# Kernel optimization log

Measured on AMD Instinct MI355X. Metric: run time of the kernel, lower is better.

Reference implementation:

```python
import jax, jax.numpy as jnp
import numpy as np

B, T, D_IN, HID, D_OUT = 16, 4096, 256, 512, 256


def setup_inputs() -> dict:
    key = jax.random.key(0)
    k0, k1, k2, k3 = jax.random.split(key, 4)
    x = jax.random.normal(k0, (B, T, D_IN), dtype=jnp.float32)
    # nn.Linear default init ~ U(-1/sqrt(fan_in), 1/sqrt(fan_in)); approximate with scaled normal
    W_in = jax.random.normal(k1, (HID, D_IN), dtype=jnp.float32) / np.sqrt(D_IN)
    # hidden_ff.weight is explicitly set to diag(rand(hid_dim)) in the module
    W_h = jnp.diag(jax.random.uniform(k2, (HID,), dtype=jnp.float32))
    W_out = jax.random.normal(k3, (D_OUT, HID), dtype=jnp.float32) / np.sqrt(HID)
    return {"x": x, "W_in": W_in, "W_h": W_h, "W_out": W_out}


def reference(x, W_in, W_h, W_out):
    # x: [B, T, D_in]; W_in: [H, D_in]; W_h: [H, H]; W_out: [D_out, H]
    xp = jnp.einsum('btd,hd->bth', x, W_in)  # input projection, [B, T, H]

    def step(h, xt):
        # h_t = x_t + h_{t-1} @ W_h^T  (linear recurrence, h_0 = 0)
        h_next = xt + h @ W_h.T
        return h_next, h_next

    h0 = jnp.zeros((x.shape[0], W_h.shape[0]), dtype=x.dtype)
    _, hs = jax.lax.scan(step, h0, jnp.swapaxes(xp, 0, 1))  # hs: [T, B, H]
    hs = jnp.swapaxes(hs, 0, 1)  # [B, T, H]
    return jnp.einsum('bth,oh->bto', hs, W_out)  # [B, T, D_out]
```

## Files before the change

### kernel.cpp

```cpp
#include <hip/hip_runtime.h>
#include <hip/hip_bf16.h>
#include <stdint.h>

#define BATCH 16
#define SEQT  4096
#define DIN   256
#define HID   512
#define DOUT  256
#define M_TOT 65536
#define CLEN  128
#define NCHUNK 32

typedef short bf16x8 __attribute__((ext_vector_type(8)));
typedef float f32x4  __attribute__((ext_vector_type(4)));
typedef unsigned short u16;
typedef unsigned short u16x4 __attribute__((ext_vector_type(4)));
typedef unsigned int uint32;

__device__ __forceinline__ void ld_lds16(const void* g, void* l) {
    __builtin_amdgcn_global_load_lds(
        (const __attribute__((address_space(1))) void*)g,
        (__attribute__((address_space(3))) void*)l, 16, 0, 0);
}

__device__ __forceinline__ u16 f2bf_rne(float f) {
    uint32 v = __float_as_uint(f);
    v += 0x7FFFu + ((v >> 16) & 1u);
    return (u16)(v >> 16);
}

__device__ __forceinline__ float bf2f(u16 s) {
    return __uint_as_float((uint32)s << 16);
}

__device__ __forceinline__ void splitf(float f, u16& hi, u16& lo) {
    const uint32 u = __float_as_uint(f);
    hi = (u16)(u >> 16);
    lo = f2bf_rne(f - __uint_as_float(u & 0xFFFF0000u));
}

__global__ __launch_bounds__(256) void prep(
        const float* __restrict__ Wh, const float* __restrict__ Win,
        const float* __restrict__ Wout, float* __restrict__ wdiag,
        float* __restrict__ wpow, u16* __restrict__ Winhi,
        u16* __restrict__ Winlo, u16* __restrict__ Wouthi,
        u16* __restrict__ Woutlo) {
    const int bid = blockIdx.x, tid = threadIdx.x;
    if (bid == 0) {
        for (int h = tid; h < HID; h += 256) {
            const float wv = Wh[(size_t)h * HID + h];
            wdiag[h] = wv;
            float p = 1.f;
            for (int t = 0; t < CLEN; ++t) { p *= wv; wpow[t * HID + h] = p; }
        }
    } else if (bid <= 128) {
        const int f4 = (bid - 1) * 256 + tid;
        const f32x4 v = *(const f32x4*)(Win + (size_t)f4 * 4);
        u16x4 hv, lv;
#pragma unroll
        for (int k = 0; k < 4; ++k) { u16 a, b; splitf(v[k], a, b); hv[k] = a; lv[k] = b; }
        *(u16x4*)(Winhi + (size_t)f4 * 4) = hv;
        *(u16x4*)(Winlo + (size_t)f4 * 4) = lv;
    } else {
        const int f4 = (bid - 129) * 256 + tid;
        const f32x4 v = *(const f32x4*)(Wout + (size_t)f4 * 4);
        u16x4 hv, lv;
#pragma unroll
        for (int k = 0; k < 4; ++k) { u16 a, b; splitf(v[k], a, b); hv[k] = a; lv[k] = b; }
        *(u16x4*)(Wouthi + (size_t)f4 * 4) = hv;
        *(u16x4*)(Woutlo + (size_t)f4 * 4) = lv;
    }
}

__global__ __launch_bounds__(256, 2) void gemm1_scan(
        const float* __restrict__ X, const u16* __restrict__ Whi,
        const u16* __restrict__ Wlo, u16* __restrict__ localbf,
        float* __restrict__ L, const float* __restrict__ wdiag) {
    __shared__ __align__(16) char smem[66048];
    u16*   Ah  = (u16*)smem;
    u16*   Al  = (u16*)(smem + 16384);
    u16*   Bh  = (u16*)(smem + 32768);
    u16*   Bl  = (u16*)(smem + 49152);
    u16*   stb = (u16*)smem;
    float* xw  = (float*)(smem + 65536);

    const int tid  = threadIdx.x;
    const int w    = tid >> 6;
    const int lane = tid & 63;

    const int bid  = blockIdx.x;
    const int xcd  = bid & 7;
    const int slot = bid >> 3;
    const int mBase = (xcd * 64 + (slot >> 2)) * 128;
    const int nBase = (slot & 3) * 128;

    const int wr = w >> 1, wc = w & 1;
    const int fr = lane & 15;
    const int kg = lane >> 4;

    const int bRow = lane >> 3;
    const int bCol = ((lane & 7) ^ bRow) * 8;

    f32x4 acc[4][4];
#pragma unroll
    for (int i = 0; i < 4; ++i)
#pragma unroll
        for (int j = 0; j < 4; ++j) acc[i][j] = (f32x4){0.f, 0.f, 0.f, 0.f};

    for (int k0 = 0; k0 < DIN; k0 += 64) {
#pragma unroll
        for (int i = 0; i < 4; ++i) {
            const int c = w * 4 + i;
            const int r = c * 8 + bRow;
            ld_lds16(Whi + (size_t)(nBase + r) * DIN + k0 + bCol, Bh + c * 512);
            ld_lds16(Wlo + (size_t)(nBase + r) * DIN + k0 + bCol, Bl + c * 512);
        }
#pragma unroll
        for (int it = 0; it < 4; ++it) {
            const int idx = it * 256 + tid;
            const int r  = idx >> 3;
            const int gl = idx & 7;
            const float* src = X + (size_t)(mBase + r) * DIN + k0 + gl * 8;
            const f32x4 v0 = *(const f32x4*)(src);
            const f32x4 v1 = *(const f32x4*)(src + 4);
            bf16x8 h8, l8;
#pragma unroll
            for (int e = 0; e < 4; ++e) {
                u16 a, b;
                splitf(v0[e], a, b); h8[e] = (short)a; l8[e] = (short)b;
                splitf(v1[e], a, b); h8[e + 4] = (short)a; l8[e + 4] = (short)b;
            }
            const int phys = r * 64 + ((gl ^ (r & 7)) * 8);
            *(bf16x8*)(Ah + phys) = h8;
            *(bf16x8*)(Al + phys) = l8;
        }
        __syncthreads();
#pragma unroll
        for (int ks = 0; ks < 2; ++ks) {
            const int colE = ks * 32 + kg * 8;
            bf16x8 ah[4], al[4], bh[4], bl[4];
#pragma unroll
            for (int f = 0; f < 4; ++f) {
                const int ra = wr * 64 + f * 16 + fr;
                const int pa = ra * 64 + (colE ^ ((fr & 7) << 3));
                ah[f] = *(const bf16x8*)(Ah + pa);
                al[f] = *(const bf16x8*)(Al + pa);
                const int rb = wc * 64 + f * 16 + fr;
                const int pb = rb * 64 + (colE ^ ((fr & 7) << 3));
                bh[f] = *(const bf16x8*)(Bh + pb);
                bl[f] = *(const bf16x8*)(Bl + pb);
            }
#pragma unroll
            for (int i = 0; i < 4; ++i)
#pragma unroll
                for (int j = 0; j < 4; ++j) {
                    acc[i][j] = __builtin_amdgcn_mfma_f32_16x16x32_bf16(ah[i], bh[j], acc[i][j], 0, 0, 0);
                    acc[i][j] = __builtin_amdgcn_mfma_f32_16x16x32_bf16(ah[i], bl[j], acc[i][j], 0, 0, 0);
                    acc[i][j] = __builtin_amdgcn_mfma_f32_16x16x32_bf16(al[i], bh[j], acc[i][j], 0, 0, 0);
                }
        }
        __syncthreads();
    }

    float w1[4], w2[4], w3[4], w4[4], w8[4], w16[4];
#pragma unroll
    for (int j = 0; j < 4; ++j) {
        const float wv = wdiag[nBase + wc * 64 + j * 16 + fr];
        w1[j] = wv; w2[j] = wv * wv; w3[j] = w2[j] * wv; w4[j] = w2[j] * w2[j];
        w8[j] = w4[j] * w4[j]; w16[j] = w8[j] * w8[j];
    }
    float Bst[4] = {0.f, 0.f, 0.f, 0.f};
#pragma unroll
    for (int i = 0; i < 4; ++i) {
#pragma unroll
        for (int j = 0; j < 4; ++j) {
            const float l0 = acc[i][j][0];
            const float l1 = fmaf(w1[j], l0, acc[i][j][1]);
            const float l2 = fmaf(w1[j], l1, acc[i][j][2]);
            const float l3 = fmaf(w1[j], l2, acc[i][j][3]);
            const float x0 = __shfl(l3, fr);
            const float x1 = __shfl(l3, fr + 16);
            const float x2 = __shfl(l3, fr + 32);
            const float x3 = __shfl(l3, fr + 48);
            float s = Bst[j];
            float S = s;
            s = fmaf(w4[j], s, x0); S = (kg == 1) ? s : S;
            s = fmaf(w4[j], s, x1); S = (kg == 2) ? s : S;
            s = fmaf(w4[j], s, x2); S = (kg == 3) ? s : S;
            s = fmaf(w4[j], s, x3);
            Bst[j] = s;
            acc[i][j][0] = fmaf(w1[j], S, l0);
            acc[i][j][1] = fmaf(w2[j], S, l1);
            acc[i][j][2] = fmaf(w3[j], S, l2);
            acc[i][j][3] = fmaf(w4[j], S, l3);
        }
    }
    if (wr == 0 && kg == 0) {
#pragma unroll
        for (int j = 0; j < 4; ++j) xw[wc * 64 + j * 16 + fr] = Bst[j];
    }
    __syncthreads();
    if (wr == 1) {
        const int cI = (mBase >> 7) & (NCHUNK - 1);
        const int bI = mBase >> 12;
#pragma unroll
        for (int j = 0; j < 4; ++j) {
            const float cin = xw[wc * 64 + j * 16 + fr];
            float wkg = 1.f;
            if (kg & 1) wkg *= w4[j];
            if (kg & 2) wkg *= w8[j];
            float f = wkg;
#pragma unroll
            for (int i = 0; i < 4; ++i) {
                const float g = f * cin;
                acc[i][j][0] = fmaf(w1[j], g, acc[i][j][0]);
                acc[i][j][1] = fmaf(w2[j], g, acc[i][j][1]);
                acc[i][j][2] = fmaf(w3[j], g, acc[i][j][2]);
                acc[i][j][3] = fmaf(w4[j], g, acc[i][j][3]);
                f *= w16[j];
            }
            if (kg == 0) {
                const float w32 = w16[j] * w16[j];
                const float w64 = w32 * w32;
                L[(cI * BATCH + bI) * HID + nBase + wc * 64 + j * 16 + fr]
                    = fmaf(w64, cin, Bst[j]);
            }
        }
    }
#pragma unroll
    for (int i = 0; i < 4; ++i)
#pragma unroll
        for (int j = 0; j < 4; ++j)
#pragma unroll
            for (int rg = 0; rg < 4; ++rg)
                stb[(wr * 64 + i * 16 + kg * 4 + rg) * 132
                    + wc * 64 + j * 16 + fr] = f2bf_rne(acc[i][j][rg]);
    __syncthreads();

    {
        const int rr2 = tid >> 4;
        const int cl  = (tid & 15) * 8;
#pragma unroll
        for (int p = 0; p < 8; ++p) {
            const int row = p * 16 + rr2;
            const bf16x8 v = *(const bf16x8*)(stb + row * 132 + cl);
            *(bf16x8*)(localbf + (size_t)(mBase + row) * HID + nBase + cl) = v;
        }
    }
}

__global__ __launch_bounds__(256) void scan_carry(
        const float* __restrict__ L, const float* __restrict__ wpow,
        float* __restrict__ carry) {
    const int idx = blockIdx.x * 256 + threadIdx.x;
    const int h = idx & (HID - 1);
    const int b = idx >> 9;
    const float wf = wpow[(CLEN - 1) * HID + h];
    float H = 0.f;
    for (int c = 0; c < NCHUNK; ++c) {
        const int o = (c * BATCH + b) * HID + h;
        carry[o] = H;
        H = fmaf(wf, H, L[o]);
    }
}

__global__ __launch_bounds__(256, 2) void gemm2_fix(
        const u16* __restrict__ localbf, const u16* __restrict__ Bhi_g,
        const u16* __restrict__ Blo_g, const float* __restrict__ wpow,
        const float* __restrict__ carry, float* __restrict__ C) {
    __shared__ __align__(16) char smem[65536];
    u16* Ah = (u16*)smem;
    u16* Al = (u16*)(smem + 16384);
    u16* Bh = (u16*)(smem + 32768);
    u16* Bl = (u16*)(smem + 49152);

    const int tid  = threadIdx.x;
    const int w    = tid >> 6;
    const int lane = tid & 63;

    const int bid  = blockIdx.x;
    const int xcd  = bid & 7;
    const int slot = bid >> 3;
    const int mBase = (xcd * 64 + (slot >> 1)) * 128;
    const int nBase = (slot & 1) * 128;

    const int wr = w >> 1, wc = w & 1;
    const int fr = lane & 15;
    const int kg = lane >> 4;

    const int bRow = lane >> 3;
    const int bCol = ((lane & 7) ^ bRow) * 8;

    const int cI = (mBase >> 7) & (NCHUNK - 1);
    const int bI = mBase >> 12;
    const float* crow = carry + (size_t)(cI * BATCH + bI) * HID;

    f32x4 acc[4][4];
#pragma unroll
    for (int i = 0; i < 4; ++i)
#pragma unroll
        for (int j = 0; j < 4; ++j) acc[i][j] = (f32x4){0.f, 0.f, 0.f, 0.f};

    for (int k0 = 0; k0 < HID; k0 += 64) {
#pragma unroll
        for (int i = 0; i < 4; ++i) {
            const int c = w * 4 + i;
            const int r2 = c * 8 + bRow;
            ld_lds16(Bhi_g + (size_t)(nBase + r2) * HID + k0 + bCol, Bh + c * 512);
            ld_lds16(Blo_g + (size_t)(nBase + r2) * HID + k0 + bCol, Bl + c * 512);
        }
#pragma unroll
        for (int it = 0; it < 4; ++it) {
            const int idx = it * 256 + tid;
            const int r  = idx >> 3;
            const int gl = idx & 7;
            const int gm = mBase + r;
            const size_t col = (size_t)(k0 + gl * 8);
            const bf16x8 lv = *(const bf16x8*)(localbf + (size_t)gm * HID + col);
            const f32x4 p0 = *(const f32x4*)(wpow + (size_t)r * HID + col);
            const f32x4 p1 = *(const f32x4*)(wpow + (size_t)r * HID + col + 4);
            const f32x4 c0 = *(const f32x4*)(crow + col);
            const f32x4 c1 = *(const f32x4*)(crow + col + 4);
            bf16x8 h8, l8;
#pragma unroll
            for (int e = 0; e < 4; ++e) {
                const float f0 = fmaf(p0[e], c0[e], bf2f((u16)lv[e]));
                const float f1 = fmaf(p1[e], c1[e], bf2f((u16)lv[e + 4]));
                u16 a, b;
                splitf(f0, a, b); h8[e] = (short)a; l8[e] = (short)b;
                splitf(f1, a, b); h8[e + 4] = (short)a; l8[e + 4] = (short)b;
            }
            const int phys = r * 64 + ((gl ^ (r & 7)) * 8);
            *(bf16x8*)(Ah + phys) = h8;
            *(bf16x8*)(Al + phys) = l8;
        }
        __syncthreads();
#pragma unroll
        for (int ks = 0; ks < 2; ++ks) {
            const int colE = ks * 32 + kg * 8;
            bf16x8 ah[4], al[4], bh[4], bl[4];
#pragma unroll
            for (int f = 0; f < 4; ++f) {
                const int ra = wr * 64 + f * 16 + fr;
                const int pa = ra * 64 + (colE ^ ((fr & 7) << 3));
                ah[f] = *(const bf16x8*)(Ah + pa);
                al[f] = *(const bf16x8*)(Al + pa);
                const int rb = wc * 64 + f * 16 + fr;
                const int pb = rb * 64 + (colE ^ ((fr & 7) << 3));
                bh[f] = *(const bf16x8*)(Bh + pb);
                bl[f] = *(const bf16x8*)(Bl + pb);
            }
#pragma unroll
            for (int i = 0; i < 4; ++i)
#pragma unroll
                for (int j = 0; j < 4; ++j) {
                    acc[i][j] = __builtin_amdgcn_mfma_f32_16x16x32_bf16(ah[i], bh[j], acc[i][j], 0, 0, 0);
                    acc[i][j] = __builtin_amdgcn_mfma_f32_16x16x32_bf16(ah[i], bl[j], acc[i][j], 0, 0, 0);
                    acc[i][j] = __builtin_amdgcn_mfma_f32_16x16x32_bf16(al[i], bh[j], acc[i][j], 0, 0, 0);
                }
        }
        __syncthreads();
    }

#pragma unroll
    for (int i = 0; i < 4; ++i) {
        const size_t row0 = (size_t)mBase + wr * 64 + i * 16 + kg * 4;
#pragma unroll
        for (int j = 0; j < 4; ++j) {
            const int col = nBase + wc * 64 + j * 16 + fr;
#pragma unroll
            for (int rg = 0; rg < 4; ++rg)
                C[(row0 + rg) * DOUT + col] = acc[i][j][rg];
        }
    }
}

extern "C" void kernel_launch(void* const* d_in, const int* in_sizes, int n_in,
                              void* d_out, int out_size, void* d_ws, size_t ws_size,
                              hipStream_t stream) {
    const float* x     = (const float*)d_in[0];
    const float* W_in  = (const float*)d_in[1];
    const float* W_h   = (const float*)d_in[2];
    const float* W_out = (const float*)d_in[3];
    float* out = (float*)d_out;

    char* ws = (char*)d_ws;
    u16*   localbf = (u16*)(ws);
    float* L       = (float*)(ws + 134217728);
    float* carry   = (float*)(ws + 135266304);
    float* wpow    = (float*)(ws + 136314880);
    float* wdiag   = (float*)(ws + 136577024);
    u16*   Winhi   = (u16*)(ws + 136579072);
    u16*   Winlo   = (u16*)(ws + 136841216);
    u16*   Wouthi  = (u16*)(ws + 137103360);
    u16*   Woutlo  = (u16*)(ws + 137365504);

    prep<<<257, 256, 0, stream>>>(W_h, W_in, W_out, wdiag, wpow,
                                  Winhi, Winlo, Wouthi, Woutlo);
    gemm1_scan<<<2048, 256, 0, stream>>>(x, Winhi, Winlo, localbf, L, wdiag);
    scan_carry<<<32, 256, 0, stream>>>(L, wpow, carry);
    gemm2_fix<<<1024, 256, 0, stream>>>(localbf, Wouthi, Woutlo, wpow, carry, out);
}
```

Before: 134.8 us.

## Widen gemm1 tile to the full hidden width so X is split once

The input-projection+scan kernel now has each 512-thread block compute a 128x512 tile covering the whole hidden dimension, instead of a 128x128 tile with four blocks per row stripe. This removes the fourfold redundant global reads of X and its fp32-to-hi/lo bf16 splitting. The K step drops to 32 and the full W_in hi/lo slice is staged in LDS each step. The bf16 output is written back in two half-width passes through LDS. In exchange, each thread holds twice as many accumulators (128 floats), which raises register pressure, and LDS use per block grows, which may limit occupancy.

```diff
diff --git a/kernel.cpp b/kernel.cpp
--- a/kernel.cpp
+++ b/kernel.cpp
@@ -72,17 +72,17 @@
     }
 }
 
-__global__ __launch_bounds__(256, 2) void gemm1_scan(
+__global__ __launch_bounds__(512, 2) void gemm1_scan(
         const float* __restrict__ X, const u16* __restrict__ Whi,
         const u16* __restrict__ Wlo, u16* __restrict__ localbf,
         float* __restrict__ L, const float* __restrict__ wdiag) {
-    __shared__ __align__(16) char smem[66048];
+    __shared__ __align__(16) char smem[81920];
     u16*   Ah  = (u16*)smem;
-    u16*   Al  = (u16*)(smem + 16384);
-    u16*   Bh  = (u16*)(smem + 32768);
+    u16*   Al  = (u16*)(smem + 8192);
+    u16*   Bh  = (u16*)(smem + 16384);
     u16*   Bl  = (u16*)(smem + 49152);
     u16*   stb = (u16*)smem;
-    float* xw  = (float*)(smem + 65536);
+    float* xw  = (float*)(smem + 67584);
 
     const int tid  = threadIdx.x;
     const int w    = tid >> 6;
@@ -91,36 +91,37 @@
     const int bid  = blockIdx.x;
     const int xcd  = bid & 7;
     const int slot = bid >> 3;
-    const int mBase = (xcd * 64 + (slot >> 2)) * 128;
-    const int nBase = (slot & 3) * 128;
-
-    const int wr = w >> 1, wc = w & 1;
+    const int mBase = (xcd * 64 + slot) * 128;
+
+    const int wr = w >> 2;
+    const int wc = w & 3;
     const int fr = lane & 15;
     const int kg = lane >> 4;
 
-    const int bRow = lane >> 3;
-    const int bCol = ((lane & 7) ^ bRow) * 8;
-
-    f32x4 acc[4][4];
+    const int r_a = tid >> 2;
+    const int g_a = (tid & 3) ^ (r_a & 3);
+
+    const int rl  = lane >> 2;
+    const int pg  = lane & 3;
+    const int lgb = pg ^ (rl & 3);
+
+    f32x4 acc[4][8];
 #pragma unroll
     for (int i = 0; i < 4; ++i)
 #pragma unroll
-        for (int j = 0; j < 4; ++j) acc[i][j] = (f32x4){0.f, 0.f, 0.f, 0.f};
-
-    for (int k0 = 0; k0 < DIN; k0 += 64) {
-#pragma unroll
-        for (int i = 0; i < 4; ++i) {
-            const int c = w * 4 + i;
-            const int r = c * 8 + bRow;
-            ld_lds16(Whi + (size_t)(nBase + r) * DIN + k0 + bCol, Bh + c * 512);
-            ld_lds16(Wlo + (size_t)(nBase + r) * DIN + k0 + bCol, Bl + c * 512);
-        }
-#pragma unroll
-        for (int it = 0; it < 4; ++it) {
-            const int idx = it * 256 + tid;
-            const int r  = idx >> 3;
-            const int gl = idx & 7;
-            const float* src = X + (size_t)(mBase + r) * DIN + k0 + gl * 8;
+        for (int j = 0; j < 8; ++j) acc[i][j] = (f32x4){0.f, 0.f, 0.f, 0.f};
+
+    for (int kk = 0; kk < 8; ++kk) {
+        const int k0 = kk * 32;
+#pragma unroll
+        for (int q = 0; q < 4; ++q) {
+            const int c = w * 4 + q;
+            const int row = c * 16 + rl;
+            ld_lds16(Whi + (size_t)row * DIN + k0 + lgb * 8, Bh + c * 512);
+            ld_lds16(Wlo + (size_t)row * DIN + k0 + lgb * 8, Bl + c * 512);
+        }
+        {
+            const float* src = X + (size_t)(mBase + r_a) * DIN + k0 + (tid & 3) * 8;
             const f32x4 v0 = *(const f32x4*)(src);
             const f32x4 v1 = *(const f32x4*)(src + 4);
             bf16x8 h8, l8;
@@ -130,122 +131,125 @@
                 splitf(v0[e], a, b); h8[e] = (short)a; l8[e] = (short)b;
                 splitf(v1[e], a, b); h8[e + 4] = (short)a; l8[e + 4] = (short)b;
             }
-            const int phys = r * 64 + ((gl ^ (r & 7)) * 8);
-            *(bf16x8*)(Ah + phys) = h8;
-            *(bf16x8*)(Al + phys) = l8;
-        }
-        __syncthreads();
-#pragma unroll
-        for (int ks = 0; ks < 2; ++ks) {
-            const int colE = ks * 32 + kg * 8;
-            bf16x8 ah[4], al[4], bh[4], bl[4];
-#pragma unroll
-            for (int f = 0; f < 4; ++f) {
-                const int ra = wr * 64 + f * 16 + fr;
-                const int pa = ra * 64 + (colE ^ ((fr & 7) << 3));
-                ah[f] = *(const bf16x8*)(Ah + pa);
-                al[f] = *(const bf16x8*)(Al + pa);
-                const int rb = wc * 64 + f * 16 + fr;
-                const int pb = rb * 64 + (colE ^ ((fr & 7) << 3));
-                bh[f] = *(const bf16x8*)(Bh + pb);
-                bl[f] = *(const bf16x8*)(Bl + pb);
-            }
-#pragma unroll
-            for (int i = 0; i < 4; ++i)
-#pragma unroll
-                for (int j = 0; j < 4; ++j) {
-                    acc[i][j] = __builtin_amdgcn_mfma_f32_16x16x32_bf16(ah[i], bh[j], acc[i][j], 0, 0, 0);
-                    acc[i][j] = __builtin_amdgcn_mfma_f32_16x16x32_bf16(ah[i], bl[j], acc[i][j], 0, 0, 0);
-                    acc[i][j] = __builtin_amdgcn_mfma_f32_16x16x32_bf16(al[i], bh[j], acc[i][j], 0, 0, 0);
-                }
-        }
-        __syncthreads();
-    }
-
-    float w1[4], w2[4], w3[4], w4[4], w8[4], w16[4];
-#pragma unroll
-    for (int j = 0; j < 4; ++j) {
-        const float wv = wdiag[nBase + wc * 64 + j * 16 + fr];
-        w1[j] = wv; w2[j] = wv * wv; w3[j] = w2[j] * wv; w4[j] = w2[j] * w2[j];
-        w8[j] = w4[j] * w4[j]; w16[j] = w8[j] * w8[j];
-    }
-    float Bst[4] = {0.f, 0.f, 0.f, 0.f};
-#pragma unroll
-    for (int i = 0; i < 4; ++i) {
-#pragma unroll
-        for (int j = 0; j < 4; ++j) {
+            *(bf16x8*)(Ah + r_a * 32 + g_a * 8) = h8;
+            *(bf16x8*)(Al + r_a * 32 + g_a * 8) = l8;
+        }
+        __syncthreads();
+
+        const int gsw = (fr & 3);
+        bf16x8 ah[4], al[4];
+#pragma unroll
+        for (int i = 0; i < 4; ++i) {
+            const int sa = (wr * 64 + i * 16 + fr) * 32 + ((kg ^ gsw) * 8);
+            ah[i] = *(const bf16x8*)(Ah + sa);
+            al[i] = *(const bf16x8*)(Al + sa);
+        }
+#pragma unroll
+        for (int j = 0; j < 8; ++j) {
+            const int sb = (wc * 128 + j * 16 + fr) * 32 + ((kg ^ gsw) * 8);
+            const bf16x8 bh = *(const bf16x8*)(Bh + sb);
+            const bf16x8 bl = *(const bf16x8*)(Bl + sb);
+#pragma unroll
+            for (int i = 0; i < 4; ++i) {
+                acc[i][j] = __builtin_amdgcn_mfma_f32_16x16x32_bf16(ah[i], bh, acc[i][j], 0, 0, 0);
+                acc[i][j] = __builtin_amdgcn_mfma_f32_16x16x32_bf16(ah[i], bl, acc[i][j], 0, 0, 0);
+                acc[i][j] = __builtin_amdgcn_mfma_f32_16x16x32_bf16(al[i], bh, acc[i][j], 0, 0, 0);
+            }
+        }
+        __syncthreads();
+    }
+
+    float Bst[8];
+#pragma unroll
+    for (int j = 0; j < 8; ++j) Bst[j] = 0.f;
+
+#pragma unroll
+    for (int j = 0; j < 8; ++j) {
+        const float w1 = wdiag[wc * 128 + j * 16 + fr];
+        const float w2 = w1 * w1, w3 = w2 * w1, w4 = w2 * w2;
+#pragma unroll
+        for (int i = 0; i < 4; ++i) {
             const float l0 = acc[i][j][0];
-            const float l1 = fmaf(w1[j], l0, acc[i][j][1]);
-            const float l2 = fmaf(w1[j], l1, acc[i][j][2]);
-            const float l3 = fmaf(w1[j], l2, acc[i][j][3]);
+            const float l1 = fmaf(w1, l0, acc[i][j][1]);
+            const float l2 = fmaf(w1, l1, acc[i][j][2]);
+            const float l3 = fmaf(w1, l2, acc[i][j][3]);
             const float x0 = __shfl(l3, fr);
             const float x1 = __shfl(l3, fr + 16);
             const float x2 = __shfl(l3, fr + 32);
             const float x3 = __shfl(l3, fr + 48);
             float s = Bst[j];
             float S = s;
-            s = fmaf(w4[j], s, x0); S = (kg == 1) ? s : S;
-            s = fmaf(w4[j], s, x1); S = (kg == 2) ? s : S;
-            s = fmaf(w4[j], s, x2); S = (kg == 3) ? s : S;
-            s = fmaf(w4[j], s, x3);
+            s = fmaf(w4, s, x0); S = (kg == 1) ? s : S;
+            s = fmaf(w4, s, x1); S = (kg == 2) ? s : S;
+            s = fmaf(w4, s, x2); S = (kg == 3) ? s : S;
+            s = fmaf(w4, s, x3);
             Bst[j] = s;
-            acc[i][j][0] = fmaf(w1[j], S, l0);
-            acc[i][j][1] = fmaf(w2[j], S, l1);
-            acc[i][j][2] = fmaf(w3[j], S, l2);
-            acc[i][j][3] = fmaf(w4[j], S, l3);
+            acc[i][j][0] = fmaf(w1, S, l0);
+            acc[i][j][1] = fmaf(w2, S, l1);
+            acc[i][j][2] = fmaf(w3, S, l2);
+            acc[i][j][3] = fmaf(w4, S, l3);
         }
     }
     if (wr == 0 && kg == 0) {
 #pragma unroll
-        for (int j = 0; j < 4; ++j) xw[wc * 64 + j * 16 + fr] = Bst[j];
+        for (int j = 0; j < 8; ++j) xw[wc * 128 + j * 16 + fr] = Bst[j];
     }
     __syncthreads();
     if (wr == 1) {
         const int cI = (mBase >> 7) & (NCHUNK - 1);
         const int bI = mBase >> 12;
 #pragma unroll
-        for (int j = 0; j < 4; ++j) {
-            const float cin = xw[wc * 64 + j * 16 + fr];
+        for (int j = 0; j < 8; ++j) {
+            const int col = wc * 128 + j * 16 + fr;
+            const float w1 = wdiag[col];
+            const float w2 = w1 * w1, w3 = w2 * w1, w4 = w2 * w2;
+            const float w8 = w4 * w4, w16 = w8 * w8;
+            const float cin = xw[col];
             float wkg = 1.f;
-            if (kg & 1) wkg *= w4[j];
-            if (kg & 2) wkg *= w8[j];
+            if (kg & 1) wkg *= w4;
+            if (kg & 2) wkg *= w8;
             float f = wkg;
 #pragma unroll
             for (int i = 0; i < 4; ++i) {
                 const float g = f * cin;
-                acc[i][j][0] = fmaf(w1[j], g, acc[i][j][0]);
-                acc[i][j][1] = fmaf(w2[j], g, acc[i][j][1]);
-                acc[i][j][2] = fmaf(w3[j], g, acc[i][j][2]);
-                acc[i][j][3] = fmaf(w4[j], g, acc[i][j][3]);
-                f *= w16[j];
+                acc[i][j][0] = fmaf(w1, g, acc[i][j][0]);
+                acc[i][j][1] = fmaf(w2, g, acc[i][j][1]);
+                acc[i][j][2] = fmaf(w3, g, acc[i][j][2]);
+                acc[i][j][3] = fmaf(w4, g, acc[i][j][3]);
+                f *= w16;
             }
             if (kg == 0) {
-                const float w32 = w16[j] * w16[j];
+                const float w32 = w16 * w16;
                 const float w64 = w32 * w32;
-                L[(cI * BATCH + bI) * HID + nBase + wc * 64 + j * 16 + fr]
-                    = fmaf(w64, cin, Bst[j]);
-            }
-        }
-    }
-#pragma unroll
-    for (int i = 0; i < 4; ++i)
-#pragma unroll
-        for (int j = 0; j < 4; ++j)
-#pragma unroll
-            for (int rg = 0; rg < 4; ++rg)
-                stb[(wr * 64 + i * 16 + kg * 4 + rg) * 132
-                    + wc * 64 + j * 16 + fr] = f2bf_rne(acc[i][j][rg]);
+                L[(cI * BATCH + bI) * HID + col] = fmaf(w64, cin, Bst[j]);
+            }
+        }
+    }
     __syncthreads();
 
-    {
-        const int rr2 = tid >> 4;
-        const int cl  = (tid & 15) * 8;
-#pragma unroll
-        for (int p = 0; p < 8; ++p) {
-            const int row = p * 16 + rr2;
-            const bf16x8 v = *(const bf16x8*)(stb + row * 132 + cl);
-            *(bf16x8*)(localbf + (size_t)(mBase + row) * HID + nBase + cl) = v;
-        }
+#pragma unroll
+    for (int pass = 0; pass < 2; ++pass) {
+        if ((wc >> 1) == pass) {
+            const int cb = (wc & 1) * 128;
+#pragma unroll
+            for (int i = 0; i < 4; ++i)
+#pragma unroll
+                for (int j = 0; j < 8; ++j)
+#pragma unroll
+                    for (int rg = 0; rg < 4; ++rg)
+                        stb[(wr * 64 + i * 16 + kg * 4 + rg) * 264
+                            + cb + j * 16 + fr] = f2bf_rne(acc[i][j][rg]);
+        }
+        __syncthreads();
+#pragma unroll
+        for (int it = 0; it < 8; ++it) {
+            const int idx = it * 512 + tid;
+            const int row = idx >> 5, g = idx & 31;
+            const bf16x8 v = *(const bf16x8*)(stb + row * 264 + g * 8);
+            *(bf16x8*)(localbf + (size_t)(mBase + row) * HID
+                       + pass * 256 + g * 8) = v;
+        }
+        __syncthreads();
     }
 }
 
@@ -397,7 +401,7 @@
 
     prep<<<257, 256, 0, stream>>>(W_h, W_in, W_out, wdiag, wpow,
                                   Winhi, Winlo, Wouthi, Woutlo);
-    gemm1_scan<<<2048, 256, 0, stream>>>(x, Winhi, Winlo, localbf, L, wdiag);
+    gemm1_scan<<<512, 512, 0, stream>>>(x, Winhi, Winlo, localbf, L, wdiag);
     scan_carry<<<32, 256, 0, stream>>>(L, wpow, carry);
     gemm2_fix<<<1024, 256, 0, stream>>>(localbf, Wouthi, Woutlo, wpow, carry, out);
 }
```

Result: slower. 172.4 us (+27.9%).

## Widen gemm1 tile to 128x256 with 512 threads and K-step 32

Applied to the files above, without the earlier changes.

The first GEMM kernel now runs 8 waves per block over a 128x256 output tile, so each X row tile is converted to bf16 hi/lo only twice instead of four times across N. The K loop steps by 32 instead of 64 to fit the larger B tile in shared memory, and the XOR swizzle is dropped for a plain row layout. The trade-off is more sync barriers per K, possible LDS bank conflicts from the unswizzled layout, and fewer blocks in flight.

```diff
diff --git a/kernel.cpp b/kernel.cpp
--- a/kernel.cpp
+++ b/kernel.cpp
@@ -72,17 +72,17 @@
     }
 }
 
-__global__ __launch_bounds__(256, 2) void gemm1_scan(
+__global__ __launch_bounds__(512, 2) void gemm1_scan(
         const float* __restrict__ X, const u16* __restrict__ Whi,
         const u16* __restrict__ Wlo, u16* __restrict__ localbf,
         float* __restrict__ L, const float* __restrict__ wdiag) {
-    __shared__ __align__(16) char smem[66048];
+    __shared__ __align__(16) char smem[69632];
     u16*   Ah  = (u16*)smem;
-    u16*   Al  = (u16*)(smem + 16384);
-    u16*   Bh  = (u16*)(smem + 32768);
-    u16*   Bl  = (u16*)(smem + 49152);
+    u16*   Al  = (u16*)(smem + 8192);
+    u16*   Bh  = (u16*)(smem + 16384);
+    u16*   Bl  = (u16*)(smem + 32768);
     u16*   stb = (u16*)smem;
-    float* xw  = (float*)(smem + 65536);
+    float* xw  = (float*)(smem + 67584);
 
     const int tid  = threadIdx.x;
     const int w    = tid >> 6;
@@ -91,15 +91,19 @@
     const int bid  = blockIdx.x;
     const int xcd  = bid & 7;
     const int slot = bid >> 3;
-    const int mBase = (xcd * 64 + (slot >> 2)) * 128;
-    const int nBase = (slot & 3) * 128;
-
-    const int wr = w >> 1, wc = w & 1;
+    const int mBase = (xcd * 64 + (slot >> 1)) * 128;
+    const int nBase = (slot & 1) * 256;
+
+    const int wr = w >> 2;
+    const int wc = w & 3;
     const int fr = lane & 15;
     const int kg = lane >> 4;
 
-    const int bRow = lane >> 3;
-    const int bCol = ((lane & 7) ^ bRow) * 8;
+    const int r_a = tid >> 2;
+    const int g_a = tid & 3;
+
+    const int rl = lane >> 2;
+    const int pg = lane & 3;
 
     f32x4 acc[4][4];
 #pragma unroll
@@ -107,20 +111,17 @@
 #pragma unroll
         for (int j = 0; j < 4; ++j) acc[i][j] = (f32x4){0.f, 0.f, 0.f, 0.f};
 
-    for (int k0 = 0; k0 < DIN; k0 += 64) {
-#pragma unroll
-        for (int i = 0; i < 4; ++i) {
-            const int c = w * 4 + i;
-            const int r = c * 8 + bRow;
-            ld_lds16(Whi + (size_t)(nBase + r) * DIN + k0 + bCol, Bh + c * 512);
-            ld_lds16(Wlo + (size_t)(nBase + r) * DIN + k0 + bCol, Bl + c * 512);
-        }
-#pragma unroll
-        for (int it = 0; it < 4; ++it) {
-            const int idx = it * 256 + tid;
-            const int r  = idx >> 3;
-            const int gl = idx & 7;
-            const float* src = X + (size_t)(mBase + r) * DIN + k0 + gl * 8;
+    for (int kk = 0; kk < 8; ++kk) {
+        const int k0 = kk * 32;
+#pragma unroll
+        for (int q = 0; q < 2; ++q) {
+            const int c = w * 2 + q;
+            const int row = nBase + c * 16 + rl;
+            ld_lds16(Whi + (size_t)row * DIN + k0 + pg * 8, Bh + c * 512);
+            ld_lds16(Wlo + (size_t)row * DIN + k0 + pg * 8, Bl + c * 512);
+        }
+        {
+            const float* src = X + (size_t)(mBase + r_a) * DIN + k0 + g_a * 8;
             const f32x4 v0 = *(const f32x4*)(src);
             const f32x4 v1 = *(const f32x4*)(src + 4);
             bf16x8 h8, l8;
@@ -130,34 +131,29 @@
                 splitf(v0[e], a, b); h8[e] = (short)a; l8[e] = (short)b;
                 splitf(v1[e], a, b); h8[e + 4] = (short)a; l8[e + 4] = (short)b;
             }
-            const int phys = r * 64 + ((gl ^ (r & 7)) * 8);
-            *(bf16x8*)(Ah + phys) = h8;
-            *(bf16x8*)(Al + phys) = l8;
+            *(bf16x8*)(Ah + r_a * 32 + g_a * 8) = h8;
+            *(bf16x8*)(Al + r_a * 32 + g_a * 8) = l8;
         }
         __syncthreads();
-#pragma unroll
-        for (int ks = 0; ks < 2; ++ks) {
-            const int colE = ks * 32 + kg * 8;
-            bf16x8 ah[4], al[4], bh[4], bl[4];
-#pragma unroll
-            for (int f = 0; f < 4; ++f) {
-                const int ra = wr * 64 + f * 16 + fr;
-                const int pa = ra * 64 + (colE ^ ((fr & 7) << 3));
-                ah[f] = *(const bf16x8*)(Ah + pa);
-                al[f] = *(const bf16x8*)(Al + pa);
-                const int rb = wc * 64 + f * 16 + fr;
-                const int pb = rb * 64 + (colE ^ ((fr & 7) << 3));
-                bh[f] = *(const bf16x8*)(Bh + pb);
-                bl[f] = *(const bf16x8*)(Bl + pb);
-            }
-#pragma unroll
-            for (int i = 0; i < 4; ++i)
-#pragma unroll
-                for (int j = 0; j < 4; ++j) {
-                    acc[i][j] = __builtin_amdgcn_mfma_f32_16x16x32_bf16(ah[i], bh[j], acc[i][j], 0, 0, 0);
-                    acc[i][j] = __builtin_amdgcn_mfma_f32_16x16x32_bf16(ah[i], bl[j], acc[i][j], 0, 0, 0);
-                    acc[i][j] = __builtin_amdgcn_mfma_f32_16x16x32_bf16(al[i], bh[j], acc[i][j], 0, 0, 0);
-                }
+
+        bf16x8 ah[4], al[4];
+#pragma unroll
+        for (int i = 0; i < 4; ++i) {
+            const int sa = (wr * 64 + i * 16 + fr) * 32 + kg * 8;
+            ah[i] = *(const bf16x8*)(Ah + sa);
+            al[i] = *(const bf16x8*)(Al + sa);
+        }
+#pragma unroll
+        for (int j = 0; j < 4; ++j) {
+            const int sb = (wc * 64 + j * 16 + fr) * 32 + kg * 8;
+            const bf16x8 bh = *(const bf16x8*)(Bh + sb);
+            const bf16x8 bl = *(const bf16x8*)(Bl + sb);
+#pragma unroll
+            for (int i = 0; i < 4; ++i) {
+                acc[i][j] = __builtin_amdgcn_mfma_f32_16x16x32_bf16(ah[i], bh, acc[i][j], 0, 0, 0);
+                acc[i][j] = __builtin_amdgcn_mfma_f32_16x16x32_bf16(ah[i], bl, acc[i][j], 0, 0, 0);
+                acc[i][j] = __builtin_amdgcn_mfma_f32_16x16x32_bf16(al[i], bh, acc[i][j], 0, 0, 0);
+            }
         }
         __syncthreads();
     }
@@ -227,25 +223,24 @@
             }
         }
     }
+    __syncthreads();
+
 #pragma unroll
     for (int i = 0; i < 4; ++i)
 #pragma unroll
         for (int j = 0; j < 4; ++j)
 #pragma unroll
             for (int rg = 0; rg < 4; ++rg)
-                stb[(wr * 64 + i * 16 + kg * 4 + rg) * 132
+                stb[(wr * 64 + i * 16 + kg * 4 + rg) * 264
                     + wc * 64 + j * 16 + fr] = f2bf_rne(acc[i][j][rg]);
     __syncthreads();
 
-    {
-        const int rr2 = tid >> 4;
-        const int cl  = (tid & 15) * 8;
-#pragma unroll
-        for (int p = 0; p < 8; ++p) {
-            const int row = p * 16 + rr2;
-            const bf16x8 v = *(const bf16x8*)(stb + row * 132 + cl);
-            *(bf16x8*)(localbf + (size_t)(mBase + row) * HID + nBase + cl) = v;
-        }
+#pragma unroll
+    for (int it = 0; it < 8; ++it) {
+        const int idx = it * 512 + tid;
+        const int row = idx >> 5, g = idx & 31;
+        const bf16x8 v = *(const bf16x8*)(stb + row * 264 + g * 8);
+        *(bf16x8*)(localbf + (size_t)(mBase + row) * HID + nBase + g * 8) = v;
     }
 }
 
@@ -397,7 +392,7 @@
 
     prep<<<257, 256, 0, stream>>>(W_h, W_in, W_out, wdiag, wpow,
                                   Winhi, Winlo, Wouthi, Woutlo);
-    gemm1_scan<<<2048, 256, 0, stream>>>(x, Winhi, Winlo, localbf, L, wdiag);
+    gemm1_scan<<<1024, 512, 0, stream>>>(x, Winhi, Winlo, localbf, L, wdiag);
     scan_carry<<<32, 256, 0, stream>>>(L, wpow, carry);
     gemm2_fix<<<1024, 256, 0, stream>>>(localbf, Wouthi, Woutlo, wpow, carry, out);
 }
```

New measurement: 147.1 us, median of 2. 9.1% more time.
